# Kernel optimization log

Hardware: AMD Instinct MI355X
Metric: run time of the kernel (lower is better)

The kernel has to match this reference:

```python
import jax, jax.numpy as jnp
import numpy as np

N = 50000   # nodes
E = 800000  # edges (before self loops)
D = 128     # hidden_channels (= input_dim here)
G = 64      # graphs in batch
NEG_SLOPE = 0.2


def setup_inputs() -> dict:
    key = jax.random.key(0)
    ks = jax.random.split(key, 16)
    s = 1.0 / np.sqrt(D)
    inp = {
        "x": jax.random.normal(ks[0], (N, D), jnp.float32),
        "edge_index": jax.random.randint(ks[1], (2, E), 0, N, dtype=jnp.int32),
        "batch": jnp.sort(jax.random.randint(ks[2], (N,), 0, G, dtype=jnp.int32)),
        "lin_in_w": jax.random.normal(ks[3], (D, D), jnp.float32) * s,
        "lin_in_b": jnp.zeros((D,), jnp.float32),
        "w1": jax.random.normal(ks[4], (D, D), jnp.float32) * s,
        "asrc1": jax.random.normal(ks[5], (D,), jnp.float32) * s,
        "adst1": jax.random.normal(ks[6], (D,), jnp.float32) * s,
        "b1": jnp.zeros((D,), jnp.float32),
        "w2": jax.random.normal(ks[7], (D, D), jnp.float32) * s,
        "asrc2": jax.random.normal(ks[8], (D,), jnp.float32) * s,
        "adst2": jax.random.normal(ks[9], (D,), jnp.float32) * s,
        "b2": jnp.zeros((D,), jnp.float32),
        "out_w": jax.random.normal(ks[10], (D, 1), jnp.float32) * s,
        "out_b": jnp.zeros((1,), jnp.float32),
    }
    return inp


def gat_conv(h_in, src, dst, W, a_src, a_dst, b):
    # h: [N, D] projected features (heads=1, concat irrelevant)
    h = h_in @ W
    alpha_s = (h * a_src).sum(-1)  # [N]
    alpha_d = (h * a_dst).sum(-1)  # [N]
    e = jax.nn.leaky_relu(alpha_s[src] + alpha_d[dst], NEG_SLOPE)  # [E+N]
    # segment softmax over destination nodes
    m = jax.ops.segment_max(e, dst, num_segments=N)
    e = jnp.exp(e - m[dst])
    denom = jax.ops.segment_sum(e, dst, num_segments=N)
    alpha = e / denom[dst]
    out = jax.ops.segment_sum(alpha[:, None] * h[src], dst, num_segments=N)
    return out + b


def reference(x, edge_index, batch, lin_in_w, lin_in_b,
              w1, asrc1, adst1, b1, w2, asrc2, adst2, b2, out_w, out_b):
    loops = jnp.arange(N, dtype=edge_index.dtype)
    src = jnp.concatenate([edge_index[0], loops])  # add_self_loops=True
    dst = jnp.concatenate([edge_index[1], loops])
    h = x @ lin_in_w + lin_in_b
    h = jax.nn.relu(gat_conv(h, src, dst, w1, asrc1, adst1, b1))
    h = jax.nn.relu(gat_conv(h, src, dst, w2, asrc2, adst2, b2))
    # global mean pool over graphs
    cnt = jax.ops.segment_sum(jnp.ones((N,), h.dtype), batch, num_segments=G)
    pooled = jax.ops.segment_sum(h, batch, num_segments=G) / cnt[:, None]
    return pooled @ out_w + out_b
```

## Files before the change

### kernel.cpp

```cpp
#include <hip/hip_runtime.h>
#include <hip/hip_bf16.h>

#define NEG_SLOPE 0.2f
#define BSHIFT 8
#define MAXBUCK 256
#define LDA 136

typedef __attribute__((ext_vector_type(8))) short bfrag;
typedef __attribute__((ext_vector_type(4))) float ffrag;

static __device__ __forceinline__ float b2f(unsigned short u){
  return __uint_as_float(((unsigned int)u) << 16);
}
static __device__ __forceinline__ unsigned short f2b16(float f){
  unsigned int u = __float_as_uint(f);
  return (unsigned short)((u + 0x7fffu + ((u >> 16) & 1u)) >> 16);
}
static __device__ __forceinline__ unsigned int pack_bf2(float a, float b){
  return (unsigned int)f2b16(a) | ((unsigned int)f2b16(b) << 16);
}

__global__ __launch_bounds__(256) void k_init(const int* __restrict__ batch,
    int* bcnt, int* gs, int* ge, int n){
  int i = blockIdx.x * 256 + threadIdx.x;
  if(i < MAXBUCK) bcnt[i] = 0;
  if(i < n){
    int g = batch[i];
    if(i == 0){
      gs[g] = 0;
    } else {
      int gp = batch[i - 1];
      if(gp != g){ gs[g] = i; ge[gp] = i; }
    }
    if(i == n - 1) ge[g] = n;
  }
}

__global__ __launch_bounds__(256) void k_prep(const float* __restrict__ lin_w,
    const float* __restrict__ lin_b, const float* __restrict__ w1,
    const float* __restrict__ w2, unsigned short* __restrict__ Wtc,
    float* __restrict__ bc, unsigned short* __restrict__ Wt2){
  if(blockIdx.x == 4){
    int c = threadIdx.x;
    if(c < 128){
      float s = 0.f;
      for(int k = 0; k < 128; k++) s += lin_b[k] * w1[k * 128 + c];
      bc[c] = s;
    }
    return;
  }
  if(blockIdx.x == 5){
    const int t = threadIdx.x;
    #pragma unroll
    for(int i = 0; i < 16; i++){
      int idx = t + i * 256;
      int k = idx >> 5, n0 = (idx & 31) * 4;
      float4 v = ((const float4*)w2)[idx];
      Wt2[(n0+0) * 128 + k] = f2b16(v.x);
// ... 260 lines not shown
  const int b = blockIdx.x;
  const int n0 = b << BSHIFT;
  const int t = threadIdx.x;
  const int lo = boff[b];
  const int cnt = bcnt[b];
  dcnt[t] = 0;
  __syncthreads();
  for(int j = t; j < cnt; j += 256){
    uint2 ed = staged[lo + j];
    atomicAdd(&dcnt[(int)(ed.y) - n0], 1);
  }
  __syncthreads();
  int v = dcnt[t];
  doff[t] = v;
  __syncthreads();
  for(int off = 1; off < (1 << BSHIFT); off <<= 1){
    int x = (t >= off) ? doff[t - off] : 0;
    __syncthreads();
    doff[t] += x;
    __syncthreads();
  }
  int excl = doff[t] - v;
  int i = n0 + t;
  if(i < n) rowptr[i] = lo + excl;
  dcnt[t] = excl;
  __syncthreads();
  for(int j = t; j < cnt; j += 256){
    uint2 ed = staged[lo + j];
    int pos = atomicAdd(&dcnt[(int)(ed.y) - n0], 1);
    esrc[lo + pos] = (int)ed.x;
  }
}

__global__ __launch_bounds__(256) void k_gat(const unsigned int* __restrict__ hb,
    const int* __restrict__ rowptr, const int* __restrict__ esrc,
    const float* __restrict__ a_s, const float* __restrict__ a_d,
    const float* __restrict__ bias, unsigned int* __restrict__ hb_out, int n, int Etot){
  __shared__ uint2 pairs[4][64];
  const int t = threadIdx.x;
  int w = (blockIdx.x * 256 + t) >> 6;
  const int lane = t & 63;
  const int wvid = t >> 6;
  if(w >= n) return;
  int s0 = rowptr[w], s1 = rowptr[w + 1];
  s0 = max(0, min(s0, Etot));
  s1 = max(s0, min(s1, Etot));
  const int deg = s1 - s0;
  const float adv = a_d[w];
  float2 acc0 = make_float2(0.f, 0.f), acc1 = make_float2(0.f, 0.f);
  float2 acc2 = make_float2(0.f, 0.f), acc3 = make_float2(0.f, 0.f);

  if(deg <= 64){
    int srcl = 0;
    if(lane < deg){
      srcl = esrc[s0 + lane];
      srcl = ((unsigned)srcl < (unsigned)n) ? srcl : 0;
    }
    int i0 = __shfl(srcl, 0), i1 = __shfl(srcl, 1);
    int i2 = __shfl(srcl, 2), i3 = __shfl(srcl, 3);
    int i4 = __shfl(srcl, 4), i5 = __shfl(srcl, 5);
    int i6 = __shfl(srcl, 6), i7 = __shfl(srcl, 7);
    unsigned int u0 = hb[(((unsigned)i0) << 6) + lane];
    unsigned int u1 = hb[(((unsigned)i1) << 6) + lane];
    unsigned int u2 = hb[(((unsigned)i2) << 6) + lane];
    unsigned int u3 = hb[(((unsigned)i3) << 6) + lane];
    unsigned int u4 = hb[(((unsigned)i4) << 6) + lane];
    unsigned int u5 = hb[(((unsigned)i5) << 6) + lane];
    unsigned int u6 = hb[(((unsigned)i6) << 6) + lane];
    unsigned int u7 = hb[(((unsigned)i7) << 6) + lane];
    float e = -1e30f;
    if(lane < deg){
      float v = a_s[srcl] + adv;
      e = v > 0.f ? v : NEG_SLOPE * v;
    }
    float m = e;
    #pragma unroll
    for(int o = 32; o; o >>= 1) m = fmaxf(m, __shfl_xor(m, o));
    float wgt = (lane < deg) ? __expf(e - m) : 0.f;
    float den = wgt;
    #pragma unroll
    for(int o = 32; o; o >>= 1) den += __shfl_xor(den, o);
    float winv = (den > 0.f) ? wgt / den : 0.f;
    pairs[wvid][lane] = make_uint2((unsigned)srcl, __float_as_uint(winv));
    float w0 = __shfl(winv, 0), w1 = __shfl(winv, 1);
    float w2 = __shfl(winv, 2), w3 = __shfl(winv, 3);
    float w4 = __shfl(winv, 4), w5 = __shfl(winv, 5);
    float w6 = __shfl(winv, 6), w7 = __shfl(winv, 7);
    acc0.x += w0 * b2f((unsigned short)(u0 & 0xffffu)); acc0.y += w0 * b2f((unsigned short)(u0 >> 16));
    acc1.x += w1 * b2f((unsigned short)(u1 & 0xffffu)); acc1.y += w1 * b2f((unsigned short)(u1 >> 16));
    acc2.x += w2 * b2f((unsigned short)(u2 & 0xffffu)); acc2.y += w2 * b2f((unsigned short)(u2 >> 16));
    acc3.x += w3 * b2f((unsigned short)(u3 & 0xffffu)); acc3.y += w3 * b2f((unsigned short)(u3 >> 16));
    acc0.x += w4 * b2f((unsigned short)(u4 & 0xffffu)); acc0.y += w4 * b2f((unsigned short)(u4 >> 16));
    acc1.x += w5 * b2f((unsigned short)(u5 & 0xffffu)); acc1.y += w5 * b2f((unsigned short)(u5 >> 16));
    acc2.x += w6 * b2f((unsigned short)(u6 & 0xffffu)); acc2.y += w6 * b2f((unsigned short)(u6 >> 16));
    acc3.x += w7 * b2f((unsigned short)(u7 & 0xffffu)); acc3.y += w7 * b2f((unsigned short)(u7 >> 16));
    int jj = 8;
    for(; jj + 8 <= deg; jj += 8){
      uint2 p0 = pairs[wvid][jj + 0], p1 = pairs[wvid][jj + 1];
      uint2 p2 = pairs[wvid][jj + 2], p3 = pairs[wvid][jj + 3];
      uint2 p4 = pairs[wvid][jj + 4], p5 = pairs[wvid][jj + 5];
      uint2 p6 = pairs[wvid][jj + 6], p7 = pairs[wvid][jj + 7];
      unsigned int v0 = hb[(p0.x << 6) + lane];
      unsigned int v1 = hb[(p1.x << 6) + lane];
      unsigned int v2 = hb[(p2.x << 6) + lane];
      unsigned int v3 = hb[(p3.x << 6) + lane];
      unsigned int v4 = hb[(p4.x << 6) + lane];
      unsigned int v5 = hb[(p5.x << 6) + lane];
      unsigned int v6 = hb[(p6.x << 6) + lane];
      unsigned int v7 = hb[(p7.x << 6) + lane];
      float q0 = __uint_as_float(p0.y), q1 = __uint_as_float(p1.y);
      float q2 = __uint_as_float(p2.y), q3 = __uint_as_float(p3.y);
      float q4 = __uint_as_float(p4.y), q5 = __uint_as_float(p5.y);
      float q6 = __uint_as_float(p6.y), q7 = __uint_as_float(p7.y);
      acc0.x += q0 * b2f((unsigned short)(v0 & 0xffffu)); acc0.y += q0 * b2f((unsigned short)(v0 >> 16));
      acc1.x += q1 * b2f((unsigned short)(v1 & 0xffffu)); acc1.y += q1 * b2f((unsigned short)(v1 >> 16));
      acc2.x += q2 * b2f((unsigned short)(v2 & 0xffffu)); acc2.y += q2 * b2f((unsigned short)(v2 >> 16));
      acc3.x += q3 * b2f((unsigned short)(v3 & 0xffffu)); acc3.y += q3 * b2f((unsigned short)(v3 >> 16));
      acc0.x += q4 * b2f((unsigned short)(v4 & 0xffffu)); acc0.y += q4 * b2f((unsigned short)(v4 >> 16));
      acc1.x += q5 * b2f((unsigned short)(v5 & 0xffffu)); acc1.y += q5 * b2f((unsigned short)(v5 >> 16));
      acc2.x += q6 * b2f((unsigned short)(v6 & 0xffffu)); acc2.y += q6 * b2f((unsigned short)(v6 >> 16));
      acc3.x += q7 * b2f((unsigned short)(v7 & 0xffffu)); acc3.y += q7 * b2f((unsigned short)(v7 >> 16));
    }
    if(jj + 4 <= deg){
      uint2 p0 = pairs[wvid][jj + 0], p1 = pairs[wvid][jj + 1];
      uint2 p2 = pairs[wvid][jj + 2], p3 = pairs[wvid][jj + 3];
      unsigned int v0 = hb[(p0.x << 6) + lane];
      unsigned int v1 = hb[(p1.x << 6) + lane];
      unsigned int v2 = hb[(p2.x << 6) + lane];
      unsigned int v3 = hb[(p3.x << 6) + lane];
      float q0 = __uint_as_float(p0.y), q1 = __uint_as_float(p1.y);
      float q2 = __uint_as_float(p2.y), q3 = __uint_as_float(p3.y);
      acc0.x += q0 * b2f((unsigned short)(v0 & 0xffffu)); acc0.y += q0 * b2f((unsigned short)(v0 >> 16));
      acc1.x += q1 * b2f((unsigned short)(v1 & 0xffffu)); acc1.y += q1 * b2f((unsigned short)(v1 >> 16));
      acc2.x += q2 * b2f((unsigned short)(v2 & 0xffffu)); acc2.y += q2 * b2f((unsigned short)(v2 >> 16));
      acc3.x += q3 * b2f((unsigned short)(v3 & 0xffffu)); acc3.y += q3 * b2f((unsigned short)(v3 >> 16));
      jj += 4;
    }
    for(; jj < deg; jj++){
      uint2 p = pairs[wvid][jj];
      unsigned int v = hb[(p.x << 6) + lane];
      float q = __uint_as_float(p.y);
      acc0.x += q * b2f((unsigned short)(v & 0xffffu));
      acc0.y += q * b2f((unsigned short)(v >> 16));
    }
  } else {
    float m = -1e30f;
    for(int j = s0 + lane; j < s1; j += 64){
      int s = esrc[j]; s = ((unsigned)s < (unsigned)n) ? s : 0;
      float e = a_s[s] + adv;
      e = e > 0.f ? e : NEG_SLOPE * e;
      m = fmaxf(m, e);
    }
    #pragma unroll
    for(int o = 32; o; o >>= 1) m = fmaxf(m, __shfl_xor(m, o));
    float den = 0.f;
    for(int j = s0 + lane; j < s1; j += 64){
      int s = esrc[j]; s = ((unsigned)s < (unsigned)n) ? s : 0;
      float e = a_s[s] + adv;
      e = e > 0.f ? e : NEG_SLOPE * e;
      den += __expf(e - m);
    }
    #pragma unroll
    for(int o = 32; o; o >>= 1) den += __shfl_xor(den, o);
    float inv = (den > 0.f) ? 1.f / den : 0.f;
    for(int j = s0; j < s1; j++){
      int s = esrc[j]; s = ((unsigned)s < (unsigned)n) ? s : 0;
      float e = a_s[s] + adv;
      e = e > 0.f ? e : NEG_SLOPE * e;
      float wv = __expf(e - m) * inv;
      unsigned int u = hb[(((unsigned)s) << 6) + lane];
      acc0.x += wv * b2f((unsigned short)(u & 0xffffu));
      acc0.y += wv * b2f((unsigned short)(u >> 16));
    }
  }
  float2 bl = ((const float2*)bias)[lane];
  float ox = (acc0.x + acc1.x) + (acc2.x + acc3.x) + bl.x;
  float oy = (acc0.y + acc1.y) + (acc2.y + acc3.y) + bl.y;
  ox = 0.5f * (ox + fabsf(ox));
  oy = 0.5f * (oy + fabsf(oy));
  hb_out[(size_t)w * 64 + lane] = pack_bf2(ox, oy);
}

__global__ __launch_bounds__(512) void k_poolout(const unsigned int* __restrict__ h2,
    const int* __restrict__ gs, const int* __restrict__ ge,
    const float* __restrict__ out_w, const float* __restrict__ out_b,
    float* __restrict__ out, int n){
  const int g = blockIdx.x;
  const int t = threadIdx.x;
  const int f2 = t & 63;
  const int rr = t >> 6;
  int s = gs[g], e = ge[g];
  s = max(0, min(s, n)); e = max(s, min(e, n));
  float sx = 0.f, sy = 0.f;
  for(int i = s + rr; i < e; i += 8){
    unsigned int u = h2[(size_t)i * 64 + f2];
    sx += b2f((unsigned short)(u & 0xffffu));
    sy += b2f((unsigned short)(u >> 16));
  }
  __shared__ float part[8 * 128];
  part[rr * 128 + 2 * f2]     = sx;
  part[rr * 128 + 2 * f2 + 1] = sy;
  __syncthreads();
  __shared__ float red[2];
  if(t < 128){
    float tot = 0.f;
    #pragma unroll
    for(int r = 0; r < 8; r++) tot += part[r * 128 + t];
    int c = e - s;
    float invc = (c > 0) ? 1.f / (float)c : 0.f;
    float v = tot * invc * out_w[t];
    #pragma unroll
    for(int o = 32; o; o >>= 1) v += __shfl_xor(v, o);
    if((t & 63) == 0) red[t >> 6] = v;
  }
  __syncthreads();
  if(t == 0) out[g] = red[0] + red[1] + out_b[0];
}

extern "C" void kernel_launch(void* const* d_in, const int* in_sizes, int n_in,
                              void* d_out, int out_size, void* d_ws, size_t ws_size,
                              hipStream_t stream){
  const float* x     = (const float*)d_in[0];
  const int*   ei    = (const int*)d_in[1];
  const int*   batch = (const int*)d_in[2];
  const float* lin_w = (const float*)d_in[3];
  const float* lin_b = (const float*)d_in[4];
  const float* w1    = (const float*)d_in[5];
  const float* as1   = (const float*)d_in[6];
  const float* ad1   = (const float*)d_in[7];
  const float* b1    = (const float*)d_in[8];
  const float* w2    = (const float*)d_in[9];
  const float* as2   = (const float*)d_in[10];
  const float* ad2   = (const float*)d_in[11];
  const float* b2    = (const float*)d_in[12];
  const float* ow    = (const float*)d_in[13];
  const float* ob    = (const float*)d_in[14];
  float* out = (float*)d_out;

  const int N = in_sizes[0] / 128;
  const int E = in_sizes[1] / 2;
  const int Etot = E + N;
  const int G = out_size;
  const int nbuck = (N + (1 << BSHIFT) - 1) >> BSHIFT;

  auto a16 = [](size_t v){ return (v + 15) & ~(size_t)15; };
  char* p = (char*)d_ws;
  int*   rowptr  = (int*)p;   p += a16((size_t)(N + 1) * 4);
  int*   bcnt    = (int*)p;   p += a16((size_t)MAXBUCK * 4);
  int*   boff    = (int*)p;   p += a16((size_t)MAXBUCK * 4);
  int*   bcur    = (int*)p;   p += a16((size_t)MAXBUCK * 4);
  int*   gs      = (int*)p;   p += a16((size_t)G * 4);
  int*   ge      = (int*)p;   p += a16((size_t)G * 4);
  float* alpha_s = (float*)p; p += a16((size_t)N * 4);
  float* alpha_d = (float*)p; p += a16((size_t)N * 4);
  unsigned short* Wtc = (unsigned short*)p; p += (size_t)128 * 128 * 2;
  float* bc      = (float*)p; p += (size_t)128 * 4;
  unsigned short* Wt2 = (unsigned short*)p; p += (size_t)128 * 128 * 2;
  int*   esrc    = (int*)p;   p += a16((size_t)Etot * 4);
  uint2* staged  = (uint2*)p; p += (size_t)Etot * 8;
  unsigned int* hb  = (unsigned int*)p; p += (size_t)N * 64 * 4;
  unsigned int* hb2 = (unsigned int*)p; p += (size_t)N * 64 * 4;

  const int cbl = (Etot + 4095) / 4096;
  k_init<<<(N + 255) / 256, 256, 0, stream>>>(batch, bcnt, gs, ge, N);
  k_bhist<<<cbl, 256, 0, stream>>>(ei, bcnt, E, Etot);
  k_bscan<<<1, 256, 0, stream>>>(bcnt, boff, bcur, rowptr, N, Etot);
  k_binA<<<cbl, 256, 0, stream>>>(ei, bcur, staged, E, Etot);
  k_binB<<<nbuck, 256, 0, stream>>>(staged, boff, bcnt, rowptr, esrc, N);

  k_prep<<<6, 256, 0, stream>>>(lin_w, lin_b, w1, w2, Wtc, bc, Wt2);

  const int gbl = (N + 63) / 64;
  const int wbl = (N + 3) / 4;

  k_gemm_proj<false><<<gbl, 256, 0, stream>>>(x, Wtc, as1, ad1, bc, hb, alpha_s, alpha_d, N);
  k_gat<<<wbl, 256, 0, stream>>>(hb, rowptr, esrc, alpha_s, alpha_d, b1, hb2, N, Etot);
  k_gemm_proj<true><<<gbl, 256, 0, stream>>>(hb2, Wt2, as2, ad2, nullptr, hb, alpha_s, alpha_d, N);
  k_gat<<<wbl, 256, 0, stream>>>(hb, rowptr, esrc, alpha_s, alpha_d, b2, hb2, N, Etot);
  k_poolout<<<G, 512, 0, stream>>>(hb2, gs, ge, ow, ob, out, N);
}
```

Baseline: 275.7 us.

## Fuse global mean pooling into second GAT layer and widen gather prefetch

The second GAT layer now accumulates its ReLU outputs straight into a per-graph pooled buffer with block-local segmented sums and float atomics, so it no longer writes the layer-2 features or reads them back in a separate pooling kernel. The final kernel only scales the pooled sums and takes a dot product with the output weights. Separately, the short-degree path now issues 16 neighbour row loads up front instead of 8, for more memory-level parallelism. The cost is atomic contention on 64x128 pooled floats, nondeterministic summation order, and more register pressure.

After: 276.5 us. Within noise of the previous version (+0.3%).

```diff
diff --git a/kernel.cpp b/kernel.cpp
--- a/kernel.cpp
+++ b/kernel.cpp
@@ -21,9 +21,10 @@
 }
 
 __global__ __launch_bounds__(256) void k_init(const int* __restrict__ batch,
-    int* bcnt, int* gs, int* ge, int n){
+    int* bcnt, int* gs, int* ge, float* pooled, int n, int npool){
   int i = blockIdx.x * 256 + threadIdx.x;
   if(i < MAXBUCK) bcnt[i] = 0;
+  if(i < npool) pooled[i] = 0.f;
   if(i < n){
     int g = batch[i];
     if(i == 0){
@@ -350,189 +351,240 @@
   }
 }
 
+template<bool POOL>
 __global__ __launch_bounds__(256) void k_gat(const unsigned int* __restrict__ hb,
     const int* __restrict__ rowptr, const int* __restrict__ esrc,
     const float* __restrict__ a_s, const float* __restrict__ a_d,
-    const float* __restrict__ bias, unsigned int* __restrict__ hb_out, int n, int Etot){
+    const float* __restrict__ bias, unsigned int* __restrict__ hb_out,
+    const int* __restrict__ batch, float* __restrict__ pooled, int n, int Etot){
   __shared__ uint2 pairs[4][64];
   const int t = threadIdx.x;
   int w = (blockIdx.x * 256 + t) >> 6;
   const int lane = t & 63;
   const int wvid = t >> 6;
-  if(w >= n) return;
-  int s0 = rowptr[w], s1 = rowptr[w + 1];
-  s0 = max(0, min(s0, Etot));
-  s1 = max(s0, min(s1, Etot));
-  const int deg = s1 - s0;
-  const float adv = a_d[w];
-  float2 acc0 = make_float2(0.f, 0.f), acc1 = make_float2(0.f, 0.f);
-  float2 acc2 = make_float2(0.f, 0.f), acc3 = make_float2(0.f, 0.f);
-
-  if(deg <= 64){
-    int srcl = 0;
-    if(lane < deg){
-      srcl = esrc[s0 + lane];
-      srcl = ((unsigned)srcl < (unsigned)n) ? srcl : 0;
-    }
-    int i0 = __shfl(srcl, 0), i1 = __shfl(srcl, 1);
-    int i2 = __shfl(srcl, 2), i3 = __shfl(srcl, 3);
-    int i4 = __shfl(srcl, 4), i5 = __shfl(srcl, 5);
-    int i6 = __shfl(srcl, 6), i7 = __shfl(srcl, 7);
-    unsigned int u0 = hb[(((unsigned)i0) << 6) + lane];
-    unsigned int u1 = hb[(((unsigned)i1) << 6) + lane];
-    unsigned int u2 = hb[(((unsigned)i2) << 6) + lane];
-    unsigned int u3 = hb[(((unsigned)i3) << 6) + lane];
-    unsigned int u4 = hb[(((unsigned)i4) << 6) + lane];
-    unsigned int u5 = hb[(((unsigned)i5) << 6) + lane];
-    unsigned int u6 = hb[(((unsigned)i6) << 6) + lane];
-    unsigned int u7 = hb[(((unsigned)i7) << 6) + lane];
-    float e = -1e30f;
-    if(lane < deg){
-      float v = a_s[srcl] + adv;
-      e = v > 0.f ? v : NEG_SLOPE * v;
-    }
-    float m = e;
-    #pragma unroll
-    for(int o = 32; o; o >>= 1) m = fmaxf(m, __shfl_xor(m, o));
-    float wgt = (lane < deg) ? __expf(e - m) : 0.f;
-    float den = wgt;
-    #pragma unroll
-    for(int o = 32; o; o >>= 1) den += __shfl_xor(den, o);
-    float winv = (den > 0.f) ? wgt / den : 0.f;
-    pairs[wvid][lane] = make_uint2((unsigned)srcl, __float_as_uint(winv));
-    float w0 = __shfl(winv, 0), w1 = __shfl(winv, 1);
-    float w2 = __shfl(winv, 2), w3 = __shfl(winv, 3);
-    float w4 = __shfl(winv, 4), w5 = __shfl(winv, 5);
-    float w6 = __shfl(winv, 6), w7 = __shfl(winv, 7);
-    acc0.x += w0 * b2f((unsigned short)(u0 & 0xffffu)); acc0.y += w0 * b2f((unsigned short)(u0 >> 16));
-    acc1.x += w1 * b2f((unsigned short)(u1 & 0xffffu)); acc1.y += w1 * b2f((unsigned short)(u1 >> 16));
-    acc2.x += w2 * b2f((unsigned short)(u2 & 0xffffu)); acc2.y += w2 * b2f((unsigned short)(u2 >> 16));
-    acc3.x += w3 * b2f((unsigned short)(u3 & 0xffffu)); acc3.y += w3 * b2f((unsigned short)(u3 >> 16));
-    acc0.x += w4 * b2f((unsigned short)(u4 & 0xffffu)); acc0.y += w4 * b2f((unsigned short)(u4 >> 16));
-    acc1.x += w5 * b2f((unsigned short)(u5 & 0xffffu)); acc1.y += w5 * b2f((unsigned short)(u5 >> 16));
-    acc2.x += w6 * b2f((unsigned short)(u6 & 0xffffu)); acc2.y += w6 * b2f((unsigned short)(u6 >> 16));
-    acc3.x += w7 * b2f((unsigned short)(u7 & 0xffffu)); acc3.y += w7 * b2f((unsigned short)(u7 >> 16));
-    int jj = 8;
-    for(; jj + 8 <= deg; jj += 8){
-      uint2 p0 = pairs[wvid][jj + 0], p1 = pairs[wvid][jj + 1];
-      uint2 p2 = pairs[wvid][jj + 2], p3 = pairs[wvid][jj + 3];
-      uint2 p4 = pairs[wvid][jj + 4], p5 = pairs[wvid][jj + 5];
-      uint2 p6 = pairs[wvid][jj + 6], p7 = pairs[wvid][jj + 7];
-      unsigned int v0 = hb[(p0.x << 6) + lane];
-      unsigned int v1 = hb[(p1.x << 6) + lane];
-      unsigned int v2 = hb[(p2.x << 6) + lane];
-      unsigned int v3 = hb[(p3.x << 6) + lane];
-      unsigned int v4 = hb[(p4.x << 6) + lane];
-      unsigned int v5 = hb[(p5.x << 6) + lane];
-      unsigned int v6 = hb[(p6.x << 6) + lane];
-      unsigned int v7 = hb[(p7.x << 6) + lane];
-      float q0 = __uint_as_float(p0.y), q1 = __uint_as_float(p1.y);
-      float q2 = __uint_as_float(p2.y), q3 = __uint_as_float(p3.y);
-      float q4 = __uint_as_float(p4.y), q5 = __uint_as_float(p5.y);
-      float q6 = __uint_as_float(p6.y), q7 = __uint_as_float(p7.y);
-      acc0.x += q0 * b2f((unsigned short)(v0 & 0xffffu)); acc0.y += q0 * b2f((unsigned short)(v0 >> 16));
-      acc1.x += q1 * b2f((unsigned short)(v1 & 0xffffu)); acc1.y += q1 * b2f((unsigned short)(v1 >> 16));
-      acc2.x += q2 * b2f((unsigned short)(v2 & 0xffffu)); acc2.y += q2 * b2f((unsigned short)(v2 >> 16));
-      acc3.x += q3 * b2f((unsigned short)(v3 & 0xffffu)); acc3.y += q3 * b2f((unsigned short)(v3 >> 16));
-      acc0.x += q4 * b2f((unsigned short)(v4 & 0xffffu)); acc0.y += q4 * b2f((unsigned short)(v4 >> 16));
-      acc1.x += q5 * b2f((unsigned short)(v5 & 0xffffu)); acc1.y += q5 * b2f((unsigned short)(v5 >> 16));
-      acc2.x += q6 * b2f((unsigned short)(v6 & 0xffffu)); acc2.y += q6 * b2f((unsigned short)(v6 >> 16));
-      acc3.x += q7 * b2f((unsigned short)(v7 & 0xffffu)); acc3.y += q7 * b2f((unsigned short)(v7 >> 16));
-    }
-    if(jj + 4 <= deg){
-      uint2 p0 = pairs[wvid][jj + 0], p1 = pairs[wvid][jj + 1];
-      uint2 p2 = pairs[wvid][jj + 2], p3 = pairs[wvid][jj + 3];
-      unsigned int v0 = hb[(p0.x << 6) + lane];
-      unsigned int v1 = hb[(p1.x << 6) + lane];
-      unsigned int v2 = hb[(p2.x << 6) + lane];
-      unsigned int v3 = hb[(p3.x << 6) + lane];
-      float q0 = __uint_as_float(p0.y), q1 = __uint_as_float(p1.y);
-      float q2 = __uint_as_float(p2.y), q3 = __uint_as_float(p3.y);
-      acc0.x += q0 * b2f((unsigned short)(v0 & 0xffffu)); acc0.y += q0 * b2f((unsigned short)(v0 >> 16));
-      acc1.x += q1 * b2f((unsigned short)(v1 & 0xffffu)); acc1.y += q1 * b2f((unsigned short)(v1 >> 16));
-      acc2.x += q2 * b2f((unsigned short)(v2 & 0xffffu)); acc2.y += q2 * b2f((unsigned short)(v2 >> 16));
-      acc3.x += q3 * b2f((unsigned short)(v3 & 0xffffu)); acc3.y += q3 * b2f((unsigned short)(v3 >> 16));
-      jj += 4;
-    }
-    for(; jj < deg; jj++){
-      uint2 p = pairs[wvid][jj];
-      unsigned int v = hb[(p.x << 6) + lane];
-      float q = __uint_as_float(p.y);
-      acc0.x += q * b2f((unsigned short)(v & 0xffffu));
-      acc0.y += q * b2f((unsigned short)(v >> 16));
-    }
-  } else {
-    float m = -1e30f;
-    for(int j = s0 + lane; j < s1; j += 64){
-      int s = esrc[j]; s = ((unsigned)s < (unsigned)n) ? s : 0;
-      float e = a_s[s] + adv;
-      e = e > 0.f ? e : NEG_SLOPE * e;
-      m = fmaxf(m, e);
-    }
-    #pragma unroll
-    for(int o = 32; o; o >>= 1) m = fmaxf(m, __shfl_xor(m, o));
-    float den = 0.f;
-    for(int j = s0 + lane; j < s1; j += 64){
-      int s = esrc[j]; s = ((unsigned)s < (unsigned)n) ? s : 0;
-      float e = a_s[s] + adv;
-      e = e > 0.f ? e : NEG_SLOPE * e;
-      den += __expf(e - m);
-    }
-    #pragma unroll
-    for(int o = 32; o; o >>= 1) den += __shfl_xor(den, o);
-    float inv = (den > 0.f) ? 1.f / den : 0.f;
-    for(int j = s0; j < s1; j++){
-      int s = esrc[j]; s = ((unsigned)s < (unsigned)n) ? s : 0;
-      float e = a_s[s] + adv;
-      e = e > 0.f ? e : NEG_SLOPE * e;
-      float wv = __expf(e - m) * inv;
-      unsigned int u = hb[(((unsigned)s) << 6) + lane];
-      acc0.x += wv * b2f((unsigned short)(u & 0xffffu));
-      acc0.y += wv * b2f((unsigned short)(u >> 16));
-    }
-  }
-  float2 bl = ((const float2*)bias)[lane];
-  float ox = (acc0.x + acc1.x) + (acc2.x + acc3.x) + bl.x;
-  float oy = (acc0.y + acc1.y) + (acc2.y + acc3.y) + bl.y;
-  ox = 0.5f * (ox + fabsf(ox));
-  oy = 0.5f * (oy + fabsf(oy));
-  hb_out[(size_t)w * 64 + lane] = pack_bf2(ox, oy);
-}
-
-__global__ __launch_bounds__(512) void k_poolout(const unsigned int* __restrict__ h2,
+  const bool alive = (w < n);
+  if(!POOL && !alive) return;
+  float ox = 0.f, oy = 0.f;
+  if(alive){
+    int s0 = rowptr[w], s1 = rowptr[w + 1];
+    s0 = max(0, min(s0, Etot));
+    s1 = max(s0, min(s1, Etot));
+    const int deg = s1 - s0;
+    const float adv = a_d[w];
+    float2 acc0 = make_float2(0.f, 0.f), acc1 = make_float2(0.f, 0.f);
+    float2 acc2 = make_float2(0.f, 0.f), acc3 = make_float2(0.f, 0.f);
+
+    if(deg <= 64){
+      int srcl = 0;
+      if(lane < deg){
+        srcl = esrc[s0 + lane];
+        srcl = ((unsigned)srcl < (unsigned)n) ? srcl : 0;
+      }
+      int i0 = __shfl(srcl, 0), i1 = __shfl(srcl, 1);
+      int i2 = __shfl(srcl, 2), i3 = __shfl(srcl, 3);
+      int i4 = __shfl(srcl, 4), i5 = __shfl(srcl, 5);
+      int i6 = __shfl(srcl, 6), i7 = __shfl(srcl, 7);
+      unsigned int u0 = hb[(((unsigned)i0) << 6) + lane];
+      unsigned int u1 = hb[(((unsigned)i1) << 6) + lane];
+      unsigned int u2 = hb[(((unsigned)i2) << 6) + lane];
+      unsigned int u3 = hb[(((unsigned)i3) << 6) + lane];
+      unsigned int u4 = hb[(((unsigned)i4) << 6) + lane];
+      unsigned int u5 = hb[(((unsigned)i5) << 6) + lane];
+      unsigned int u6 = hb[(((unsigned)i6) << 6) + lane];
+      unsigned int u7 = hb[(((unsigned)i7) << 6) + lane];
+      const bool hB = (deg > 8);
+      int i8, i9, i10, i11, i12, i13, i14, i15;
+      unsigned int u8, u9, u10, u11, u12, u13, u14, u15;
+      if(hB){
+        i8  = __shfl(srcl, 8);  i9  = __shfl(srcl, 9);
+        i10 = __shfl(srcl, 10); i11 = __shfl(srcl, 11);
+        i12 = __shfl(srcl, 12); i13 = __shfl(srcl, 13);
+        i14 = __shfl(srcl, 14); i15 = __shfl(srcl, 15);
+        u8  = hb[(((unsigned)i8)  << 6) + lane];
+        u9  = hb[(((unsigned)i9)  << 6) + lane];
+        u10 = hb[(((unsigned)i10) << 6) + lane];
+        u11 = hb[(((unsigned)i11) << 6) + lane];
+        u12 = hb[(((unsigned)i12) << 6) + lane];
+        u13 = hb[(((unsigned)i13) << 6) + lane];
+        u14 = hb[(((unsigned)i14) << 6) + lane];
+        u15 = hb[(((unsigned)i15) << 6) + lane];
+      }
+      float e = -1e30f;
+      if(lane < deg){
+        float v = a_s[srcl] + adv;
+        e = v > 0.f ? v : NEG_SLOPE * v;
+      }
+      float m = e;
+      #pragma unroll
+      for(int o = 32; o; o >>= 1) m = fmaxf(m, __shfl_xor(m, o));
+      float wgt = (lane < deg) ? __expf(e - m) : 0.f;
+      float den = wgt;
+      #pragma unroll
+      for(int o = 32; o; o >>= 1) den += __shfl_xor(den, o);
+      float winv = (den > 0.f) ? wgt / den : 0.f;
+      pairs[wvid][lane] = make_uint2((unsigned)srcl, __float_as_uint(winv));
+      float w0 = __shfl(winv, 0), w1 = __shfl(winv, 1);
+      float w2 = __shfl(winv, 2), w3 = __shfl(winv, 3);
+      float w4 = __shfl(winv, 4), w5 = __shfl(winv, 5);
+      float w6 = __shfl(winv, 6), w7 = __shfl(winv, 7);
+      acc0.x += w0 * b2f((unsigned short)(u0 & 0xffffu)); acc0.y += w0 * b2f((unsigned short)(u0 >> 16));
+      acc1.x += w1 * b2f((unsigned short)(u1 & 0xffffu)); acc1.y += w1 * b2f((unsigned short)(u1 >> 16));
+      acc2.x += w2 * b2f((unsigned short)(u2 & 0xffffu)); acc2.y += w2 * b2f((unsigned short)(u2 >> 16));
+      acc3.x += w3 * b2f((unsigned short)(u3 & 0xffffu)); acc3.y += w3 * b2f((unsigned short)(u3 >> 16));
+      acc0.x += w4 * b2f((unsigned short)(u4 & 0xffffu)); acc0.y += w4 * b2f((unsigned short)(u4 >> 16));
+      acc1.x += w5 * b2f((unsigned short)(u5 & 0xffffu)); acc1.y += w5 * b2f((unsigned short)(u5 >> 16));
+      acc2.x += w6 * b2f((unsigned short)(u6 & 0xffffu)); acc2.y += w6 * b2f((unsigned short)(u6 >> 16));
+      acc3.x += w7 * b2f((unsigned short)(u7 & 0xffffu)); acc3.y += w7 * b2f((unsigned short)(u7 >> 16));
+      if(hB){
+        float w8  = __shfl(winv, 8),  w9  = __shfl(winv, 9);
+        float w10 = __shfl(winv, 10), w11 = __shfl(winv, 11);
+        float w12 = __shfl(winv, 12), w13 = __shfl(winv, 13);
+        float w14 = __shfl(winv, 14), w15 = __shfl(winv, 15);
+        acc0.x += w8  * b2f((unsigned short)(u8  & 0xffffu)); acc0.y += w8  * b2f((unsigned short)(u8  >> 16));
+        acc1.x += w9  * b2f((unsigned short)(u9  & 0xffffu)); acc1.y += w9  * b2f((unsigned short)(u9  >> 16));
+        acc2.x += w10 * b2f((unsigned short)(u10 & 0xffffu)); acc2.y += w10 * b2f((unsigned short)(u10 >> 16));
+        acc3.x += w11 * b2f((unsigned short)(u11 & 0xffffu)); acc3.y += w11 * b2f((unsigned short)(u11 >> 16));
+        acc0.x += w12 * b2f((unsigned short)(u12 & 0xffffu)); acc0.y += w12 * b2f((unsigned short)(u12 >> 16));
+        acc1.x += w13 * b2f((unsigned short)(u13 & 0xffffu)); acc1.y += w13 * b2f((unsigned short)(u13 >> 16));
+        acc2.x += w14 * b2f((unsigned short)(u14 & 0xffffu)); acc2.y += w14 * b2f((unsigned short)(u14 >> 16));
+        acc3.x += w15 * b2f((unsigned short)(u15 & 0xffffu)); acc3.y += w15 * b2f((unsigned short)(u15 >> 16));
+      }
+      int jj = 16;
+      for(; jj + 8 <= deg; jj += 8){
+        uint2 p0 = pairs[wvid][jj + 0], p1 = pairs[wvid][jj + 1];
+        uint2 p2 = pairs[wvid][jj + 2], p3 = pairs[wvid][jj + 3];
+        uint2 p4 = pairs[wvid][jj + 4], p5 = pairs[wvid][jj + 5];
+        uint2 p6 = pairs[wvid][jj + 6], p7 = pairs[wvid][jj + 7];
+        unsigned int v0 = hb[(p0.x << 6) + lane];
+        unsigned int v1 = hb[(p1.x << 6) + lane];
+        unsigned int v2 = hb[(p2.x << 6) + lane];
+        unsigned int v3 = hb[(p3.x << 6) + lane];
+        unsigned int v4 = hb[(p4.x << 6) + lane];
+        unsigned int v5 = hb[(p5.x << 6) + lane];
+        unsigned int v6 = hb[(p6.x << 6) + lane];
+        unsigned int v7 = hb[(p7.x << 6) + lane];
+        float q0 = __uint_as_float(p0.y), q1 = __uint_as_float(p1.y);
+        float q2 = __uint_as_float(p2.y), q3 = __uint_as_float(p3.y);
+        float q4 = __uint_as_float(p4.y), q5 = __uint_as_float(p5.y);
+        float q6 = __uint_as_float(p6.y), q7 = __uint_as_float(p7.y);
+        acc0.x += q0 * b2f((unsigned short)(v0 & 0xffffu)); acc0.y += q0 * b2f((unsigned short)(v0 >> 16));
+        acc1.x += q1 * b2f((unsigned short)(v1 & 0xffffu)); acc1.y += q1 * b2f((unsigned short)(v1 >> 16));
+        acc2.x += q2 * b2f((unsigned short)(v2 & 0xffffu)); acc2.y += q2 * b2f((unsigned short)(v2 >> 16));
+        acc3.x += q3 * b2f((unsigned short)(v3 & 0xffffu)); acc3.y += q3 * b2f((unsigned short)(v3 >> 16));
+        acc0.x += q4 * b2f((unsigned short)(v4 & 0xffffu)); acc0.y += q4 * b2f((unsigned short)(v4 >> 16));
+        acc1.x += q5 * b2f((unsigned short)(v5 & 0xffffu)); acc1.y += q5 * b2f((unsigned short)(v5 >> 16));
+        acc2.x += q6 * b2f((unsigned short)(v6 & 0xffffu)); acc2.y += q6 * b2f((unsigned short)(v6 >> 16));
+        acc3.x += q7 * b2f((unsigned short)(v7 & 0xffffu)); acc3.y += q7 * b2f((unsigned short)(v7 >> 16));
+      }
+      if(jj + 4 <= deg){
+        uint2 p0 = pairs[wvid][jj + 0], p1 = pairs[wvid][jj + 1];
+        uint2 p2 = pairs[wvid][jj + 2], p3 = pairs[wvid][jj + 3];
+        unsigned int v0 = hb[(p0.x << 6) + lane];
+        unsigned int v1 = hb[(p1.x << 6) + lane];
+        unsigned int v2 = hb[(p2.x << 6) + lane];
+        unsigned int v3 = hb[(p3.x << 6) + lane];
+        float q0 = __uint_as_float(p0.y), q1 = __uint_as_float(p1.y);
+        float q2 = __uint_as_float(p2.y), q3 = __uint_as_float(p3.y);
+        acc0.x += q0 * b2f((unsigned short)(v0 & 0xffffu)); acc0.y += q0 * b2f((unsigned short)(v0 >> 16));
+        acc1.x += q1 * b2f((unsigned short)(v1 & 0xffffu)); acc1.y += q1 * b2f((unsigned short)(v1 >> 16));
+        acc2.x += q2 * b2f((unsigned short)(v2 & 0xffffu)); acc2.y += q2 * b2f((unsigned short)(v2 >> 16));
+        acc3.x += q3 * b2f((unsigned short)(v3 & 0xffffu)); acc3.y += q3 * b2f((unsigned short)(v3 >> 16));
+        jj += 4;
+      }
+      for(; jj < deg; jj++){
+        uint2 p = pairs[wvid][jj];
+        unsigned int v = hb[(p.x << 6) + lane];
+        float q = __uint_as_float(p.y);
+        acc0.x += q * b2f((unsigned short)(v & 0xffffu));
+        acc0.y += q * b2f((unsigned short)(v >> 16));
+      }
+    } else {
+      float m = -1e30f;
+      for(int j = s0 + lane; j < s1; j += 64){
+        int s = esrc[j]; s = ((unsigned)s < (unsigned)n) ? s : 0;
+        float e = a_s[s] + adv;
+        e = e > 0.f ? e : NEG_SLOPE * e;
+        m = fmaxf(m, e);
+      }
+      #pragma unroll
+      for(int o = 32; o; o >>= 1) m = fmaxf(m, __shfl_xor(m, o));
+      float den = 0.f;
+      for(int j = s0 + lane; j < s1; j += 64){
+        int s = esrc[j]; s = ((unsigned)s < (unsigned)n) ? s : 0;
+        float e = a_s[s] + adv;
+        e = e > 0.f ? e : NEG_SLOPE * e;
+        den += __expf(e - m);
+      }
+      #pragma unroll
+      for(int o = 32; o; o >>= 1) den += __shfl_xor(den, o);
+      float inv = (den > 0.f) ? 1.f / den : 0.f;
+      for(int j = s0; j < s1; j++){
+        int s = esrc[j]; s = ((unsigned)s < (unsigned)n) ? s : 0;
+        float e = a_s[s] + adv;
+        e = e > 0.f ? e : NEG_SLOPE * e;
+        float wv = __expf(e - m) * inv;
+        unsigned int u = hb[(((unsigned)s) << 6) + lane];
+        acc0.x += wv * b2f((unsigned short)(u & 0xffffu));
+        acc0.y += wv * b2f((unsigned short)(u >> 16));
+      }
+    }
+    float2 bl = ((const float2*)bias)[lane];
+    ox = (acc0.x + acc1.x) + (acc2.x + acc3.x) + bl.x;
+    oy = (acc0.y + acc1.y) + (acc2.y + acc3.y) + bl.y;
+    ox = 0.5f * (ox + fabsf(ox));
+    oy = 0.5f * (oy + fabsf(oy));
+    if(!POOL) hb_out[(size_t)w * 64 + lane] = pack_bf2(ox, oy);
+  }
+  if constexpr(POOL){
+    __shared__ float pox[4][128];
+    __shared__ int pg[4];
+    pox[wvid][2 * lane]     = ox;
+    pox[wvid][2 * lane + 1] = oy;
+    int gv = -1;
+    if(alive) gv = batch[w];
+    if(lane == 0) pg[wvid] = gv;
+    __syncthreads();
+    if(wvid == 0){
+      int curg = -1; float sx = 0.f, sy = 0.f;
+      #pragma unroll
+      for(int j = 0; j < 4; j++){
+        int gj = pg[j];
+        if(gj < 0) continue;
+        if(gj != curg){
+          if(curg >= 0){
+            atomicAdd(&pooled[curg * 128 + 2 * lane], sx);
+            atomicAdd(&pooled[curg * 128 + 2 * lane + 1], sy);
+          }
+          curg = gj; sx = 0.f; sy = 0.f;
+        }
+        sx += pox[j][2 * lane];
+        sy += pox[j][2 * lane + 1];
+      }
+      if(curg >= 0){
+        atomicAdd(&pooled[curg * 128 + 2 * lane], sx);
+        atomicAdd(&pooled[curg * 128 + 2 * lane + 1], sy);
+      }
+    }
+  }
+}
+
+__global__ __launch_bounds__(128) void k_out(const float* __restrict__ pooled,
     const int* __restrict__ gs, const int* __restrict__ ge,
     const float* __restrict__ out_w, const float* __restrict__ out_b,
     float* __restrict__ out, int n){
   const int g = blockIdx.x;
   const int t = threadIdx.x;
-  const int f2 = t & 63;
-  const int rr = t >> 6;
   int s = gs[g], e = ge[g];
   s = max(0, min(s, n)); e = max(s, min(e, n));
-  float sx = 0.f, sy = 0.f;
-  for(int i = s + rr; i < e; i += 8){
-    unsigned int u = h2[(size_t)i * 64 + f2];
-    sx += b2f((unsigned short)(u & 0xffffu));
-    sy += b2f((unsigned short)(u >> 16));
-  }
-  __shared__ float part[8 * 128];
-  part[rr * 128 + 2 * f2]     = sx;
-  part[rr * 128 + 2 * f2 + 1] = sy;
-  __syncthreads();
-  __shared__ float red[2];
-  if(t < 128){
-    float tot = 0.f;
-    #pragma unroll
-    for(int r = 0; r < 8; r++) tot += part[r * 128 + t];
-    int c = e - s;
-    float invc = (c > 0) ? 1.f / (float)c : 0.f;
-    float v = tot * invc * out_w[t];
-    #pragma unroll
-    for(int o = 32; o; o >>= 1) v += __shfl_xor(v, o);
-    if((t & 63) == 0) red[t >> 6] = v;
-  }
-  __syncthreads();
-  if(t == 0) out[g] = red[0] + red[1] + out_b[0];
+  int c = e - s;
+  float invc = (c > 0) ? 1.f / (float)c : 0.f;
+  float v = pooled[g * 128 + t] * invc * out_w[t];
+  #pragma unroll
+  for(int o = 32; o; o >>= 1) v += __shfl_xor(v, o);
+  __shared__ float r[2];
+  if((t & 63) == 0) r[t >> 6] = v;
+  __syncthreads();
+  if(t == 0) out[g] = r[0] + r[1] + out_b[0];
 }
 
 extern "C" void kernel_launch(void* const* d_in, const int* in_sizes, int n_in,
@@ -571,6 +623,7 @@
   int*   ge      = (int*)p;   p += a16((size_t)G * 4);
   float* alpha_s = (float*)p; p += a16((size_t)N * 4);
   float* alpha_d = (float*)p; p += a16((size_t)N * 4);
+  float* pooled  = (float*)p; p += a16((size_t)G * 128 * 4);
   unsigned short* Wtc = (unsigned short*)p; p += (size_t)128 * 128 * 2;
   float* bc      = (float*)p; p += (size_t)128 * 4;
   unsigned short* Wt2 = (unsigned short*)p; p += (size_t)128 * 128 * 2;
@@ -580,7 +633,7 @@
   unsigned int* hb2 = (unsigned int*)p; p += (size_t)N * 64 * 4;
 
   const int cbl = (Etot + 4095) / 4096;
-  k_init<<<(N + 255) / 256, 256, 0, stream>>>(batch, bcnt, gs, ge, N);
+  k_init<<<(N + 255) / 256, 256, 0, stream>>>(batch, bcnt, gs, ge, pooled, N, G * 128);
   k_bhist<<<cbl, 256, 0, stream>>>(ei, bcnt, E, Etot);
   k_bscan<<<1, 256, 0, stream>>>(bcnt, boff, bcur, rowptr, N, Etot);
   k_binA<<<cbl, 256, 0, stream>>>(ei, bcur, staged, E, Etot);
@@ -592,8 +645,10 @@
   const int wbl = (N + 3) / 4;
 
   k_gemm_proj<false><<<gbl, 256, 0, stream>>>(x, Wtc, as1, ad1, bc, hb, alpha_s, alpha_d, N);
-  k_gat<<<wbl, 256, 0, stream>>>(hb, rowptr, esrc, alpha_s, alpha_d, b1, hb2, N, Etot);
+  k_gat<false><<<wbl, 256, 0, stream>>>(hb, rowptr, esrc, alpha_s, alpha_d, b1, hb2,
+                                        nullptr, nullptr, N, Etot);
   k_gemm_proj<true><<<gbl, 256, 0, stream>>>(hb2, Wt2, as2, ad2, nullptr, hb, alpha_s, alpha_d, N);
-  k_gat<<<wbl, 256, 0, stream>>>(hb, rowptr, esrc, alpha_s, alpha_d, b2, hb2, N, Etot);
-  k_poolout<<<G, 512, 0, stream>>>(hb2, gs, ge, ow, ob, out, N);
-}
+  k_gat<true><<<wbl, 256, 0, stream>>>(hb, rowptr, esrc, alpha_s, alpha_d, b2, nullptr,
+                                       batch, pooled, N, Etot);
+  k_out<<<G, 128, 0, stream>>>(pooled, gs, ge, ow, ob, out, N);
+}
```

## Process two destination nodes per wave with half-wave uint2 gathers

Applied to the files above, without the earlier changes.

The GAT aggregation kernel now gives each wavefront two destination nodes. When both have degree at most 32, each half-wave handles one node, gathering 8-byte rows (4 bf16 features per lane) with 32-lane softmax reductions. Otherwise it falls back to the old full-wave path, run once per node in sequence. The aim is to make better use of lanes and memory transactions for low-degree nodes (average degree about 17), at the cost of divergence and serialized fallback when a high-degree node is paired.

Result: no change. 271.2 us (-1.6%).

```diff
diff --git a/kernel.cpp b/kernel.cpp
--- a/kernel.cpp
+++ b/kernel.cpp
@@ -350,24 +350,15 @@
   }
 }
 
-__global__ __launch_bounds__(256) void k_gat(const unsigned int* __restrict__ hb,
-    const int* __restrict__ rowptr, const int* __restrict__ esrc,
-    const float* __restrict__ a_s, const float* __restrict__ a_d,
-    const float* __restrict__ bias, unsigned int* __restrict__ hb_out, int n, int Etot){
-  __shared__ uint2 pairs[4][64];
-  const int t = threadIdx.x;
-  int w = (blockIdx.x * 256 + t) >> 6;
-  const int lane = t & 63;
-  const int wvid = t >> 6;
-  if(w >= n) return;
-  int s0 = rowptr[w], s1 = rowptr[w + 1];
-  s0 = max(0, min(s0, Etot));
-  s1 = max(s0, min(s1, Etot));
+static __device__ __forceinline__ void gat_fullwave(const unsigned int* __restrict__ hb,
+    const int* __restrict__ esrc, const float* __restrict__ a_s,
+    const float* __restrict__ a_d, const float* __restrict__ bias,
+    unsigned int* __restrict__ hb_out, uint2* pairs_w,
+    int w, int s0, int s1, int lane, int n){
   const int deg = s1 - s0;
   const float adv = a_d[w];
   float2 acc0 = make_float2(0.f, 0.f), acc1 = make_float2(0.f, 0.f);
   float2 acc2 = make_float2(0.f, 0.f), acc3 = make_float2(0.f, 0.f);
-
   if(deg <= 64){
     int srcl = 0;
     if(lane < deg){
@@ -399,7 +390,7 @@
     #pragma unroll
     for(int o = 32; o; o >>= 1) den += __shfl_xor(den, o);
     float winv = (den > 0.f) ? wgt / den : 0.f;
-    pairs[wvid][lane] = make_uint2((unsigned)srcl, __float_as_uint(winv));
+    pairs_w[lane] = make_uint2((unsigned)srcl, __float_as_uint(winv));
     float w0 = __shfl(winv, 0), w1 = __shfl(winv, 1);
     float w2 = __shfl(winv, 2), w3 = __shfl(winv, 3);
     float w4 = __shfl(winv, 4), w5 = __shfl(winv, 5);
@@ -414,10 +405,10 @@
     acc3.x += w7 * b2f((unsigned short)(u7 & 0xffffu)); acc3.y += w7 * b2f((unsigned short)(u7 >> 16));
     int jj = 8;
     for(; jj + 8 <= deg; jj += 8){
-      uint2 p0 = pairs[wvid][jj + 0], p1 = pairs[wvid][jj + 1];
-      uint2 p2 = pairs[wvid][jj + 2], p3 = pairs[wvid][jj + 3];
-      uint2 p4 = pairs[wvid][jj + 4], p5 = pairs[wvid][jj + 5];
-      uint2 p6 = pairs[wvid][jj + 6], p7 = pairs[wvid][jj + 7];
+      uint2 p0 = pairs_w[jj + 0], p1 = pairs_w[jj + 1];
+      uint2 p2 = pairs_w[jj + 2], p3 = pairs_w[jj + 3];
+      uint2 p4 = pairs_w[jj + 4], p5 = pairs_w[jj + 5];
+      uint2 p6 = pairs_w[jj + 6], p7 = pairs_w[jj + 7];
       unsigned int v0 = hb[(p0.x << 6) + lane];
       unsigned int v1 = hb[(p1.x << 6) + lane];
       unsigned int v2 = hb[(p2.x << 6) + lane];
@@ -439,23 +430,8 @@
       acc2.x += q6 * b2f((unsigned short)(v6 & 0xffffu)); acc2.y += q6 * b2f((unsigned short)(v6 >> 16));
       acc3.x += q7 * b2f((unsigned short)(v7 & 0xffffu)); acc3.y += q7 * b2f((unsigned short)(v7 >> 16));
     }
-    if(jj + 4 <= deg){
-      uint2 p0 = pairs[wvid][jj + 0], p1 = pairs[wvid][jj + 1];
-      uint2 p2 = pairs[wvid][jj + 2], p3 = pairs[wvid][jj + 3];
-      unsigned int v0 = hb[(p0.x << 6) + lane];
-      unsigned int v1 = hb[(p1.x << 6) + lane];
-      unsigned int v2 = hb[(p2.x << 6) + lane];
-      unsigned int v3 = hb[(p3.x << 6) + lane];
-      float q0 = __uint_as_float(p0.y), q1 = __uint_as_float(p1.y);
-      float q2 = __uint_as_float(p2.y), q3 = __uint_as_float(p3.y);
-      acc0.x += q0 * b2f((unsigned short)(v0 & 0xffffu)); acc0.y += q0 * b2f((unsigned short)(v0 >> 16));
-      acc1.x += q1 * b2f((unsigned short)(v1 & 0xffffu)); acc1.y += q1 * b2f((unsigned short)(v1 >> 16));
-      acc2.x += q2 * b2f((unsigned short)(v2 & 0xffffu)); acc2.y += q2 * b2f((unsigned short)(v2 >> 16));
-      acc3.x += q3 * b2f((unsigned short)(v3 & 0xffffu)); acc3.y += q3 * b2f((unsigned short)(v3 >> 16));
-      jj += 4;
-    }
     for(; jj < deg; jj++){
-      uint2 p = pairs[wvid][jj];
+      uint2 p = pairs_w[jj];
       unsigned int v = hb[(p.x << 6) + lane];
       float q = __uint_as_float(p.y);
       acc0.x += q * b2f((unsigned short)(v & 0xffffu));
@@ -497,6 +473,168 @@
   ox = 0.5f * (ox + fabsf(ox));
   oy = 0.5f * (oy + fabsf(oy));
   hb_out[(size_t)w * 64 + lane] = pack_bf2(ox, oy);
+}
+
+__global__ __launch_bounds__(256) void k_gat(const unsigned int* __restrict__ hb,
+    const int* __restrict__ rowptr, const int* __restrict__ esrc,
+    const float* __restrict__ a_s, const float* __restrict__ a_d,
+    const float* __restrict__ bias, unsigned int* __restrict__ hb_out, int n, int Etot){
+  __shared__ uint2 pairs[4][64];
+  const int t = threadIdx.x;
+  const int lane = t & 63;
+  const int wvid = t >> 6;
+  const int nA = blockIdx.x * 8 + wvid * 2;
+  if(nA >= n) return;
+  const int nB = nA + 1;
+  int r0 = rowptr[nA];
+  int r1 = rowptr[nA + 1];
+  int r2 = (nB < n) ? rowptr[nB + 1] : r1;
+  r0 = max(0, min(r0, Etot));
+  r1 = max(r0, min(r1, Etot));
+  r2 = max(r1, min(r2, Etot));
+  const int degA = r1 - r0, degB = r2 - r1;
+
+  if(degA <= 32 && degB <= 32){
+    const int half = lane >> 5;
+    const int hl = lane & 31;
+    const int w = nA + half;
+    const int s0 = half ? r1 : r0;
+    const int deg = half ? degB : degA;
+    const float adv = (w < n) ? a_d[w] : 0.f;
+    const uint2* hb2v = (const uint2*)hb;
+    float4 accA = make_float4(0.f, 0.f, 0.f, 0.f);
+    float4 accB = make_float4(0.f, 0.f, 0.f, 0.f);
+
+    int srcl = 0;
+    if(hl < deg){
+      srcl = esrc[s0 + hl];
+      srcl = ((unsigned)srcl < (unsigned)n) ? srcl : 0;
+    }
+    const int hb0 = lane & 32;
+    int i0 = __shfl(srcl, hb0 + 0), i1 = __shfl(srcl, hb0 + 1);
+    int i2 = __shfl(srcl, hb0 + 2), i3 = __shfl(srcl, hb0 + 3);
+    int i4 = __shfl(srcl, hb0 + 4), i5 = __shfl(srcl, hb0 + 5);
+    int i6 = __shfl(srcl, hb0 + 6), i7 = __shfl(srcl, hb0 + 7);
+    uint2 u0 = hb2v[(((unsigned)i0) << 5) + hl];
+    uint2 u1 = hb2v[(((unsigned)i1) << 5) + hl];
+    uint2 u2 = hb2v[(((unsigned)i2) << 5) + hl];
+    uint2 u3 = hb2v[(((unsigned)i3) << 5) + hl];
+    uint2 u4 = hb2v[(((unsigned)i4) << 5) + hl];
+    uint2 u5 = hb2v[(((unsigned)i5) << 5) + hl];
+    uint2 u6 = hb2v[(((unsigned)i6) << 5) + hl];
+    uint2 u7 = hb2v[(((unsigned)i7) << 5) + hl];
+    float e = -1e30f;
+    if(hl < deg){
+      float v = a_s[srcl] + adv;
+      e = v > 0.f ? v : NEG_SLOPE * v;
+    }
+    float m = e;
+    #pragma unroll
+    for(int o = 16; o; o >>= 1) m = fmaxf(m, __shfl_xor(m, o));
+    float wgt = (hl < deg) ? __expf(e - m) : 0.f;
+    float den = wgt;
+    #pragma unroll
+    for(int o = 16; o; o >>= 1) den += __shfl_xor(den, o);
+    float winv = (den > 0.f) ? wgt / den : 0.f;
+    pairs[wvid][lane] = make_uint2((unsigned)srcl, __float_as_uint(winv));
+    float w0 = __shfl(winv, hb0 + 0), w1 = __shfl(winv, hb0 + 1);
+    float w2 = __shfl(winv, hb0 + 2), w3 = __shfl(winv, hb0 + 3);
+    float w4 = __shfl(winv, hb0 + 4), w5 = __shfl(winv, hb0 + 5);
+    float w6 = __shfl(winv, hb0 + 6), w7 = __shfl(winv, hb0 + 7);
+    accA.x += w0 * b2f((unsigned short)(u0.x & 0xffffu)); accA.y += w0 * b2f((unsigned short)(u0.x >> 16));
+    accA.z += w0 * b2f((unsigned short)(u0.y & 0xffffu)); accA.w += w0 * b2f((unsigned short)(u0.y >> 16));
+    accB.x += w1 * b2f((unsigned short)(u1.x & 0xffffu)); accB.y += w1 * b2f((unsigned short)(u1.x >> 16));
+    accB.z += w1 * b2f((unsigned short)(u1.y & 0xffffu)); accB.w += w1 * b2f((unsigned short)(u1.y >> 16));
+    accA.x += w2 * b2f((unsigned short)(u2.x & 0xffffu)); accA.y += w2 * b2f((unsigned short)(u2.x >> 16));
+    accA.z += w2 * b2f((unsigned short)(u2.y & 0xffffu)); accA.w += w2 * b2f((unsigned short)(u2.y >> 16));
+    accB.x += w3 * b2f((unsigned short)(u3.x & 0xffffu)); accB.y += w3 * b2f((unsigned short)(u3.x >> 16));
+    accB.z += w3 * b2f((unsigned short)(u3.y & 0xffffu)); accB.w += w3 * b2f((unsigned short)(u3.y >> 16));
+    accA.x += w4 * b2f((unsigned short)(u4.x & 0xffffu)); accA.y += w4 * b2f((unsigned short)(u4.x >> 16));
+    accA.z += w4 * b2f((unsigned short)(u4.y & 0xffffu)); accA.w += w4 * b2f((unsigned short)(u4.y >> 16));
+    accB.x += w5 * b2f((unsigned short)(u5.x & 0xffffu)); accB.y += w5 * b2f((unsigned short)(u5.x >> 16));
+    accB.z += w5 * b2f((unsigned short)(u5.y & 0xffffu)); accB.w += w5 * b2f((unsigned short)(u5.y >> 16));
+    accA.x += w6 * b2f((unsigned short)(u6.x & 0xffffu)); accA.y += w6 * b2f((unsigned short)(u6.x >> 16));
+    accA.z += w6 * b2f((unsigned short)(u6.y & 0xffffu)); accA.w += w6 * b2f((unsigned short)(u6.y >> 16));
+    accB.x += w7 * b2f((unsigned short)(u7.x & 0xffffu)); accB.y += w7 * b2f((unsigned short)(u7.x >> 16));
+    accB.z += w7 * b2f((unsigned short)(u7.y & 0xffffu)); accB.w += w7 * b2f((unsigned short)(u7.y >> 16));
+    int jj = 8;
+    for(; jj + 8 <= deg; jj += 8){
+      uint2 p0 = pairs[wvid][hb0 + jj + 0], p1 = pairs[wvid][hb0 + jj + 1];
+      uint2 p2 = pairs[wvid][hb0 + jj + 2], p3 = pairs[wvid][hb0 + jj + 3];
+      uint2 p4 = pairs[wvid][hb0 + jj + 4], p5 = pairs[wvid][hb0 + jj + 5];
+      uint2 p6 = pairs[wvid][hb0 + jj + 6], p7 = pairs[wvid][hb0 + jj + 7];
+      uint2 v0 = hb2v[(p0.x << 5) + hl];
+      uint2 v1 = hb2v[(p1.x << 5) + hl];
+      uint2 v2 = hb2v[(p2.x << 5) + hl];
+      uint2 v3 = hb2v[(p3.x << 5) + hl];
+      uint2 v4 = hb2v[(p4.x << 5) + hl];
+      uint2 v5 = hb2v[(p5.x << 5) + hl];
+      uint2 v6 = hb2v[(p6.x << 5) + hl];
+      uint2 v7 = hb2v[(p7.x << 5) + hl];
+      float q0 = __uint_as_float(p0.y), q1 = __uint_as_float(p1.y);
+      float q2 = __uint_as_float(p2.y), q3 = __uint_as_float(p3.y);
+      float q4 = __uint_as_float(p4.y), q5 = __uint_as_float(p5.y);
+      float q6 = __uint_as_float(p6.y), q7 = __uint_as_float(p7.y);
+      accA.x += q0 * b2f((unsigned short)(v0.x & 0xffffu)); accA.y += q0 * b2f((unsigned short)(v0.x >> 16));
+      accA.z += q0 * b2f((unsigned short)(v0.y & 0xffffu)); accA.w += q0 * b2f((unsigned short)(v0.y >> 16));
+      accB.x += q1 * b2f((unsigned short)(v1.x & 0xffffu)); accB.y += q1 * b2f((unsigned short)(v1.x >> 16));
+      accB.z += q1 * b2f((unsigned short)(v1.y & 0xffffu)); accB.w += q1 * b2f((unsigned short)(v1.y >> 16));
+      accA.x += q2 * b2f((unsigned short)(v2.x & 0xffffu)); accA.y += q2 * b2f((unsigned short)(v2.x >> 16));
+      accA.z += q2 * b2f((unsigned short)(v2.y & 0xffffu)); accA.w += q2 * b2f((unsigned short)(v2.y >> 16));
+      accB.x += q3 * b2f((unsigned short)(v3.x & 0xffffu)); accB.y += q3 * b2f((unsigned short)(v3.x >> 16));
+      accB.z += q3 * b2f((unsigned short)(v3.y & 0xffffu)); accB.w += q3 * b2f((unsigned short)(v3.y >> 16));
+      accA.x += q4 * b2f((unsigned short)(v4.x & 0xffffu)); accA.y += q4 * b2f((unsigned short)(v4.x >> 16));
+      accA.z += q4 * b2f((unsigned short)(v4.y & 0xffffu)); accA.w += q4 * b2f((unsigned short)(v4.y >> 16));
+      accB.x += q5 * b2f((unsigned short)(v5.x & 0xffffu)); accB.y += q5 * b2f((unsigned short)(v5.x >> 16));
+      accB.z += q5 * b2f((unsigned short)(v5.y & 0xffffu)); accB.w += q5 * b2f((unsigned short)(v5.y >> 16));
+      accA.x += q6 * b2f((unsigned short)(v6.x & 0xffffu)); accA.y += q6 * b2f((unsigned short)(v6.x >> 16));
+      accA.z += q6 * b2f((unsigned short)(v6.y & 0xffffu)); accA.w += q6 * b2f((unsigned short)(v6.y >> 16));
+      accB.x += q7 * b2f((unsigned short)(v7.x & 0xffffu)); accB.y += q7 * b2f((unsigned short)(v7.x >> 16));
+      accB.z += q7 * b2f((unsigned short)(v7.y & 0xffffu)); accB.w += q7 * b2f((unsigned short)(v7.y >> 16));
+    }
+    if(jj + 4 <= deg){
+      uint2 p0 = pairs[wvid][hb0 + jj + 0], p1 = pairs[wvid][hb0 + jj + 1];
+      uint2 p2 = pairs[wvid][hb0 + jj + 2], p3 = pairs[wvid][hb0 + jj + 3];
+      uint2 v0 = hb2v[(p0.x << 5) + hl];
+      uint2 v1 = hb2v[(p1.x << 5) + hl];
+      uint2 v2 = hb2v[(p2.x << 5) + hl];
+      uint2 v3 = hb2v[(p3.x << 5) + hl];
+      float q0 = __uint_as_float(p0.y), q1 = __uint_as_float(p1.y);
+      float q2 = __uint_as_float(p2.y), q3 = __uint_as_float(p3.y);
+      accA.x += q0 * b2f((unsigned short)(v0.x & 0xffffu)); accA.y += q0 * b2f((unsigned short)(v0.x >> 16));
+      accA.z += q0 * b2f((unsigned short)(v0.y & 0xffffu)); accA.w += q0 * b2f((unsigned short)(v0.y >> 16));
+      accB.x += q1 * b2f((unsigned short)(v1.x & 0xffffu)); accB.y += q1 * b2f((unsigned short)(v1.x >> 16));
+      accB.z += q1 * b2f((unsigned short)(v1.y & 0xffffu)); accB.w += q1 * b2f((unsigned short)(v1.y >> 16));
+      accA.x += q2 * b2f((unsigned short)(v2.x & 0xffffu)); accA.y += q2 * b2f((unsigned short)(v2.x >> 16));
+      accA.z += q2 * b2f((unsigned short)(v2.y & 0xffffu)); accA.w += q2 * b2f((unsigned short)(v2.y >> 16));
+      accB.x += q3 * b2f((unsigned short)(v3.x & 0xffffu)); accB.y += q3 * b2f((unsigned short)(v3.x >> 16));
+      accB.z += q3 * b2f((unsigned short)(v3.y & 0xffffu)); accB.w += q3 * b2f((unsigned short)(v3.y >> 16));
+      jj += 4;
+    }
+    for(; jj < deg; jj++){
+      uint2 p = pairs[wvid][hb0 + jj];
+      uint2 v = hb2v[(p.x << 5) + hl];
+      float q = __uint_as_float(p.y);
+      accA.x += q * b2f((unsigned short)(v.x & 0xffffu)); accA.y += q * b2f((unsigned short)(v.x >> 16));
+      accA.z += q * b2f((unsigned short)(v.y & 0xffffu)); accA.w += q * b2f((unsigned short)(v.y >> 16));
+    }
+    if(w < n){
+      float4 bl = ((const float4*)bias)[hl];
+      float f0 = accA.x + accB.x + bl.x;
+      float f1 = accA.y + accB.y + bl.y;
+      float f2 = accA.z + accB.z + bl.z;
+      float f3 = accA.w + accB.w + bl.w;
+      f0 = 0.5f * (f0 + fabsf(f0));
+      f1 = 0.5f * (f1 + fabsf(f1));
+      f2 = 0.5f * (f2 + fabsf(f2));
+      f3 = 0.5f * (f3 + fabsf(f3));
+      ((uint2*)hb_out)[((size_t)w << 5) + hl] = make_uint2(pack_bf2(f0, f1), pack_bf2(f2, f3));
+    }
+  } else {
+    gat_fullwave(hb, esrc, a_s, a_d, bias, hb_out, &pairs[wvid][0], nA, r0, r1, lane, n);
+    if(nB < n)
+      gat_fullwave(hb, esrc, a_s, a_d, bias, hb_out, &pairs[wvid][0], nB, r1, r2, lane, n);
+  }
 }
 
 __global__ __launch_bounds__(512) void k_poolout(const unsigned int* __restrict__ h2,
@@ -589,7 +727,7 @@
   k_prep<<<6, 256, 0, stream>>>(lin_w, lin_b, w1, w2, Wtc, bc, Wt2);
 
   const int gbl = (N + 63) / 64;
-  const int wbl = (N + 3) / 4;
+  const int wbl = (N + 7) / 8;
 
   k_gemm_proj<false><<<gbl, 256, 0, stream>>>(x, Wtc, as1, ad1, bc, hb, alpha_s, alpha_d, N);
   k_gat<<<wbl, 256, 0, stream>>>(hb, rowptr, esrc, alpha_s, alpha_d, b1, hb2, N, Etot);
```
